# Kernel tuning notes

Measured on AMD Instinct MI355X. Metric: run time of the kernel, lower is better.

Reference implementation:

```python
import jax, jax.numpy as jnp
import numpy as np

N_HEADS = 8
WINDOW = 7

def _conv1x1(x, W, b):
    # x: [B,H,W,C]; 1x1 conv == per-pixel matmul
    return jnp.einsum('bhwc,cd->bhwd', x, W) + b

def _to_heads(t, nh):
    # [B,H,W,C] -> channels-first reshape [B, nh, C//nh, H*W] (matches tf transpose+reshape)
    B, H, W, C = t.shape
    return jnp.transpose(t, (0, 3, 1, 2)).reshape(B, nh, C // nh, H * W)

def setup_inputs() -> dict:
    key = jax.random.key(0)
    ks = jax.random.split(key, 8)
    B, H, W, C = 2, 56, 56, 256
    x = jax.random.normal(ks[0], (B, H, W, C), dtype=jnp.float32)
    s = 1.0 / np.sqrt(C)
    Wq = jax.random.normal(ks[1], (C, C), dtype=jnp.float32) * s
    bq = jnp.zeros((C,), dtype=jnp.float32)
    Wk = jax.random.normal(ks[2], (C, C), dtype=jnp.float32) * s
    bk = jnp.zeros((C,), dtype=jnp.float32)
    Wv = jax.random.normal(ks[3], (C, C), dtype=jnp.float32) * s
    bv = jnp.zeros((C,), dtype=jnp.float32)
    # original initializes gamma to 0 (output == x); use small nonzero so the
    # attention path is observable in outputs/grads
    gamma = jax.random.normal(ks[4], (1,), dtype=jnp.float32) * 0.1
    return {"x": x, "Wq": Wq, "bq": bq, "Wk": Wk, "bk": bk, "Wv": Wv, "bv": bv, "gamma": gamma}

def reference(x, Wq, bq, Wk, bk, Wv, bv, gamma):
    B, H, W, C = x.shape
    p = WINDOW // 2
    xp = jnp.pad(x, ((0, 0), (p, p), (p, p), (0, 0)), mode='reflect')  # [B,Hp,Wp,C]
    q = _to_heads(_conv1x1(x, Wq, bq), N_HEADS)    # [B,nh,dk,HW]
    k = _to_heads(_conv1x1(xp, Wk, bk), N_HEADS)   # [B,nh,dk,HpWp]
    v = _to_heads(_conv1x1(xp, Wv, bv), N_HEADS)   # [B,nh,dk,HpWp]
    energy = jnp.einsum('bhdq,bhdk->bhqk', q, k)   # [B,nh,HW,HpWp]
    attn = jax.nn.softmax(energy, axis=-1)
    out = jnp.einsum('bhdk,bhqk->bhdq', v, attn)   # [B,nh,dk,HW]
    out = out.reshape(B, C, H, W).transpose(0, 2, 3, 1)
    return gamma * out + x
```

## Files before the change

kernel.cpp:

```cpp
#include <hip/hip_runtime.h>

typedef unsigned short u16;
typedef float f32x4 __attribute__((ext_vector_type(4)));
typedef short bf16x8 __attribute__((ext_vector_type(8)));
typedef u16 u16x4 __attribute__((ext_vector_type(4)));

__device__ __forceinline__ u16 f2bf(float f) {
    unsigned u = __float_as_uint(f);
    u = (u + 0x7FFFu + ((u >> 16) & 1u)) >> 16;
    return (u16)u;
}

#define LOG2E 1.4426950408889634f

#if __has_builtin(__builtin_amdgcn_exp2f)
__device__ __forceinline__ float exp2_fast(float x) { return __builtin_amdgcn_exp2f(x); }
#else
__device__ __forceinline__ float exp2_fast(float x) { return __expf(x * 0.6931471805599453f); }
#endif

__device__ __forceinline__ unsigned pack2bf(float a, float b) {
    unsigned ua = __float_as_uint(a) + 0x8000u;
    unsigned ub = __float_as_uint(b) + 0x8000u;
#if __has_builtin(__builtin_amdgcn_perm)
    return __builtin_amdgcn_perm(ub, ua, 0x07060302u);
#else
    return ((ua >> 16) & 0xFFFFu) | (ub & 0xFFFF0000u);
#endif
}

#if __has_builtin(__builtin_amdgcn_cvt_pk_bf16_f32)
typedef __bf16 bf2_t __attribute__((ext_vector_type(2)));
__device__ __forceinline__ unsigned cvtpk(float a, float b) {
    bf2_t r = __builtin_amdgcn_cvt_pk_bf16_f32(a, b);
    return __builtin_bit_cast(unsigned, r);
}
#else
__device__ __forceinline__ unsigned cvtpk(float a, float b) { return pack2bf(a, b); }
#endif

__device__ __forceinline__ bf16x8 bc8(uint4 u) { return __builtin_bit_cast(bf16x8, u); }

#if __has_builtin(__builtin_amdgcn_global_load_lds)
typedef const __attribute__((address_space(1))) void* as1cv;
typedef __attribute__((address_space(3))) void* as3v;
__device__ __forceinline__ void dma16(const void* g, void* lds_base, int lane) {
    __builtin_amdgcn_global_load_lds((as1cv)g, (as3v)lds_base, 16, 0, 0);
}
#else
__device__ __forceinline__ void dma16(const void* g, void* lds_base, int lane) {
    *(uint4*)((char*)lds_base + lane * 16) = *(const uint4*)g;
}
#endif

#define BB 2
#define HH 56
#define SQ 3136
#define SKP 3200
#define VT_STRIDE 3200
#define CROWN 3584

#define WS_Q    0
#define WS_K    1605632
#define WS_VT   3211264
#define WS_WT   4849664
#define WS_CB   5046272

__global__ __launch_bounds__(256) void wprep_kernel(const float* __restrict__ Wq,
                                                    const float* __restrict__ Wk,
                                                    const float* __restrict__ Wv,
                                                    u16* __restrict__ wtf,
                                                    u16* __restrict__ vtb,
                                                    u16* __restrict__ crow) {
    __shared__ u16 T[64][68];
    int mode = blockIdx.z;
    const float* W = (mode == 0) ? Wq : ((mode == 1) ? Wk : Wv);
    float sc = (mode == 0) ? LOG2E : 1.0f;
    int kx = blockIdx.x * 64, dx = blockIdx.y * 64;
    int tid = threadIdx.x;
    int r16 = tid >> 4, c4 = (tid & 15) * 4;
#pragma unroll
    for (int p = 0; p < 4; ++p) {
        int kr = p * 16 + r16;
        float4 f = *(const float4*)&W[(size_t)(kx + kr) * 256 + dx + c4];
        T[kr][c4 + 0] = f2bf(f.x * sc);
        T[kr][c4 + 1] = f2bf(f.y * sc);
        T[kr][c4 + 2] = f2bf(f.z * sc);
        T[kr][c4 + 3] = f2bf(f.w * sc);
    }
    __syncthreads();
    int l16 = tid & 15, nt_loc = (tid >> 4) & 3, quad = (tid >> 6) & 3;
#pragma unroll
    for (int s_loc = 0; s_loc < 2; ++s_loc) {
        int k0 = s_loc * 32 + quad * 8;
        int d_loc = nt_loc * 16 + l16;
        u16 tmp[8];
#pragma unroll
        for (int j = 0; j < 8; ++j) tmp[j] = T[k0 + j][d_loc];
        int d = dx + d_loc;
        int nz = d >> 7, ntg = (d >> 4) & 7;
        int s = (kx >> 5) + s_loc;
        int f = (nz * 8 + s) * 8 + ntg;
        int L = quad * 16 + l16;
        *(uint4*)&wtf[(size_t)mode * 65536 + (size_t)f * 512 + (size_t)L * 8] = *(uint4*)tmp;
    }
    if (mode == 1 && kx == 0 && dx == 0) {
        for (int i = tid; i < CROWN; i += 256) {
            u16 v = 0;
            if (i < SQ) {
                int rr = i / 56, cc = i - rr * 56;
                int mr = (((rr >= 1) && (rr <= 3)) || ((rr >= 52) && (rr <= 54))) ? 2 : 1;
                int mc = (((cc >= 1) && (cc <= 3)) || ((cc >= 52) && (cc <= 54))) ? 2 : 1;
                int prod = mr * mc;
                v = (prod == 1) ? (u16)0x3F80 : ((prod == 2) ? (u16)0x4000 : (u16)0x4080);
            }
            crow[i] = v;
        }
    }
    if (mode == 2 && kx == 0 && dx == 0) {
        for (int i = tid; i < 512 * 8; i += 256) {
            int row = i >> 3, c16 = i & 7;
            *(uint4*)&vtb[(size_t)row * VT_STRIDE + SQ + c16 * 8] = (uint4){0, 0, 0, 0};
        }
    }
}

__global__ __launch_bounds__(256, 4) void proj_kernel(const float* __restrict__ x,
                                                      const u16* __restrict__ wtf,
                                                      const float* __restrict__ bq,
                                                      const float* __restrict__ bk,
                                                      const float* __restrict__ bv,
                                                      u16* __restrict__ qout,
                                                      u16* __restrict__ kout,
                                                      u16* __restrict__ vtout) {
    int mode = blockIdx.y, nz = blockIdx.z;
    int mbase = blockIdx.x * 64;
    int tid = threadIdx.x;
    int wave = tid >> 6, quad = (tid >> 4) & 3, l16 = tid & 15;
    const float* bias = (mode == 0) ? bq : ((mode == 1) ? bk : bv);
    float wsc = (mode == 0) ? LOG2E : 1.0f;
    const u16* wf = wtf + (size_t)mode * 65536 + (size_t)nz * 32768 + (size_t)(quad * 16 + l16) * 8;

    int m_a = mbase + wave * 16 + l16;
    const float* xr = x + (size_t)m_a * 256;

    f32x4 acc[8];
#pragma unroll
    for (int i = 0; i < 8; i++) acc[i] = (f32x4){0.f, 0.f, 0.f, 0.f};

#pragma unroll
    for (int s = 0; s < 8; ++s) {
        float4 f0 = *(const float4*)&xr[s * 32 + quad * 8];
        float4 f1 = *(const float4*)&xr[s * 32 + quad * 8 + 4];
        uint4 aw = (uint4){pack2bf(f0.x, f0.y), pack2bf(f0.z, f0.w),
                           pack2bf(f1.x, f1.y), pack2bf(f1.z, f1.w)};
        bf16x8 af = bc8(aw);
        if (mode == 2) {
#pragma unroll
            for (int nt = 0; nt < 8; nt++) {
                bf16x8 bfrag = *(const bf16x8*)&wf[(s * 8 + nt) * 512];
                acc[nt] = __builtin_amdgcn_mfma_f32_16x16x32_bf16(af, bfrag, acc[nt], 0, 0, 0);
            }
        } else {
#pragma unroll
            for (int nt = 0; nt < 8; nt++) {
                bf16x8 bfrag = *(const bf16x8*)&wf[(s * 8 + nt) * 512];
                acc[nt] = __builtin_amdgcn_mfma_f32_16x16x32_bf16(bfrag, af, acc[nt], 0, 0, 0);
            }
        }
    }

    if (mode == 2) {
        int mrow_base = mbase + wave * 16 + quad * 4;
        float mult[4];
#pragma unroll
        for (int p = 0; p < 4; ++p) {
            int m = mrow_base + p;
            int kp = (m >= SQ) ? m - SQ : m;
            int rr = kp / 56, cc = kp - rr * 56;
            float mr = (((rr >= 1) && (rr <= 3)) || ((rr >= 52) && (rr <= 54))) ? 2.f : 1.f;
            float mc = (((cc >= 1) && (cc <= 3)) || ((cc >= 52) && (cc <= 54))) ? 2.f : 1.f;
            mult[p] = mr * mc;
        }
#pragma unroll
        for (int nt = 0; nt < 8; nt++) {
            int c = nz * 128 + nt * 16 + l16;
            float bvv = bias[c];
#pragma unroll
            for (int p = 0; p < 4; p += 2) {
                int m = mrow_base + p;
                int bb = (m >= SQ) ? 1 : 0;
                int kp = m - bb * SQ;
                unsigned pk = pack2bf((acc[nt][p] + bvv) * mult[p],
                                      (acc[nt][p + 1] + bvv) * mult[p + 1]);
                *(unsigned*)&vtout[(size_t)(bb * 256 + c) * VT_STRIDE + kp] = pk;
            }
        }
    } else {
        u16* outp = (mode == 0) ? qout : kout;
#pragma unroll
        for (int nt = 0; nt < 8; nt++) {
            int c0 = nz * 128 + nt * 16 + quad * 4;
            float4 b4 = *(const float4*)&bias[c0];
            float v0 = acc[nt][0] + b4.x * wsc;
            float v1 = acc[nt][1] + b4.y * wsc;
            float v2 = acc[nt][2] + b4.z * wsc;
            float v3 = acc[nt][3] + b4.w * wsc;
            uint2 pk = (uint2){pack2bf(v0, v1), pack2bf(v2, v3)};
            *(uint2*)&outp[((size_t)m_a << 8) + c0] = pk;
        }
    }
}

__global__ __launch_bounds__(256, 4) void attn_kernel(const u16* __restrict__ qb,
                                                      const u16* __restrict__ kb,
                                                      const u16* __restrict__ vtb,
                                                      const u16* __restrict__ crow,
                                                      const float* __restrict__ x,
                                                      const float* __restrict__ gammap,
                                                      float* __restrict__ out) {
    __shared__ __align__(16) u16 S[19968];

    int tid = threadIdx.x;
    int th = tid >> 6, lane = tid & 63, quad = lane >> 4, l16 = lane & 15;
    int bh = blockIdx.x;
    int b = bh >> 3, h = bh & 7;
    int qsub = blockIdx.y * 64;

    bf16x8 qf[4];
#pragma unroll
    for (int i = 0; i < 4; ++i)
        qf[i] = *(const bf16x8*)&qb[((size_t)(b * SQ + qsub + i * 16 + l16) << 8) + h * 32 + quad * 8];

    const u16* kg = kb + ((size_t)(b * SQ) << 8) + h * 32;
    const u16* vg = vtb + (size_t)(b * 256 + h * 32) * VT_STRIDE;

    f32x4 o[4][2], lv[4];
#pragma unroll
    for (int i = 0; i < 4; ++i) {
        o[i][0] = (f32x4){0.f, 0.f, 0.f, 0.f};
        o[i][1] = (f32x4){0.f, 0.f, 0.f, 0.f};
        lv[i]   = (f32x4){0.f, 0.f, 0.f, 0.f};
    }

    auto stage = [&](int r_ch, int buf) {
        u16* base = &S[buf * 8192];
        int kbase = r_ch * 128;
#pragma unroll
        for (int i = 0; i < 2; ++i) {
            int g = th + i * 4;
            int grow = kbase + g * 16 + (lane & 15);
            if (grow > SQ - 1) grow = SQ - 1;
            dma16(kg + ((size_t)grow << 8) + (lane >> 4) * 8, base + g * 512, lane);
            int col = kbase + (2 * g + (lane >> 5)) * 8;
            dma16(vg + (size_t)(lane & 31) * VT_STRIDE + col, base + 4096 + g * 512, lane);
        }
    };

    int tA = th, tB = th + 4;
    int vOffA = tA * 512 + (((quad >> 1) * 32 + l16) << 3) + (quad & 1) * 4;
    int vOffB = tB * 512 + (((quad >> 1) * 32 + l16) << 3) + (quad & 1) * 4;

    auto round_body = [&](int r, int bR) {
        const u16* Kl = &S[bR * 8192];
        const u16* Vl = Kl + 4096;
        const u16* cnt = &S[16384] + r * 128;
        bf16x8 kfA = *(const bf16x8*)&Kl[tA * 512 + lane * 8];
        bf16x8 kfB = *(const bf16x8*)&Kl[tB * 512 + lane * 8];
        uint2 ca = *(const uint2*)&cnt[tA * 16 + quad * 4];
        uint2 cc = *(const uint2*)&cnt[tB * 16 + quad * 4];
        bf16x8 cf = bc8((uint4){ca.x, ca.y, cc.x, cc.y});
        uint2 wA0 = *(const uint2*)&Vl[vOffA];
        uint2 wB0 = *(const uint2*)&Vl[vOffB];
        uint2 wA1 = *(const uint2*)&Vl[vOffA + 128];
        uint2 wB1 = *(const uint2*)&Vl[vOffB + 128];
        bf16x8 V0 = bc8((uint4){wA0.x, wA0.y, wB0.x, wB0.y});
        bf16x8 V1 = bc8((uint4){wA1.x, wA1.y, wB1.x, wB1.y});

        f32x4 z = (f32x4){0.f, 0.f, 0.f, 0.f};
        f32x4 eA[4], eB[4];
#pragma unroll
        for (int i = 0; i < 4; ++i)
            eA[i] = __builtin_amdgcn_mfma_f32_16x16x32_bf16(kfA, qf[i], z, 0, 0, 0);
#pragma unroll
        for (int i = 0; i < 4; ++i)
            eB[i] = __builtin_amdgcn_mfma_f32_16x16x32_bf16(kfB, qf[i], z, 0, 0, 0);

#pragma unroll
        for (int i = 0; i < 4; ++i) {
            float pA0 = exp2_fast(eA[i][0]), pA1 = exp2_fast(eA[i][1]);
            float pA2 = exp2_fast(eA[i][2]), pA3 = exp2_fast(eA[i][3]);
            float pB0 = exp2_fast(eB[i][0]), pB1 = exp2_fast(eB[i][1]);
            float pB2 = exp2_fast(eB[i][2]), pB3 = exp2_fast(eB[i][3]);
            bf16x8 pa = bc8((uint4){cvtpk(pA0, pA1), cvtpk(pA2, pA3),
                                    cvtpk(pB0, pB1), cvtpk(pB2, pB3)});
            o[i][0] = __builtin_amdgcn_mfma_f32_16x16x32_bf16(pa, V0, o[i][0], 0, 0, 0);
            o[i][1] = __builtin_amdgcn_mfma_f32_16x16x32_bf16(pa, V1, o[i][1], 0, 0, 0);
            lv[i]   = __builtin_amdgcn_mfma_f32_16x16x32_bf16(pa, cf, lv[i], 0, 0, 0);
        }
    };

    {
#pragma unroll
        for (int e = 0; e < 2; ++e) {
            int chn = th * 2 + e;
            if (chn < 7)
                dma16(crow + chn * 512 + lane * 8, (char*)&S[16384] + chn * 1024, lane);
        }
    }
    stage(0, 0);
    __syncthreads();

    for (int r = 0; r < 25; ++r) {
        if (r + 1 < 25) {
            stage(r + 1, (r + 1) & 1);
            asm volatile("s_waitcnt vmcnt(4)" ::: "memory");
        } else {
            asm volatile("s_waitcnt vmcnt(0)" ::: "memory");
        }
        round_body(r, r & 1);
    }

    __syncthreads();

    float* mg = (float*)&S[0];
    {
        int slot = ((th & 1) * 64 + lane) * 48;
        if (th >= 2) {
#pragma unroll
            for (int i = 0; i < 4; ++i) {
                *(f32x4*)&mg[slot + i * 8]      = o[i][0];
                *(f32x4*)&mg[slot + i * 8 + 4]  = o[i][1];
                *(f32x4*)&mg[slot + 32 + i * 4] = lv[i];
            }
        }
        __syncthreads();
        if (th < 2) {
#pragma unroll
            for (int i = 0; i < 4; ++i) {
                o[i][0] += *(const f32x4*)&mg[slot + i * 8];
                o[i][1] += *(const f32x4*)&mg[slot + i * 8 + 4];
                lv[i]   += *(const f32x4*)&mg[slot + 32 + i * 4];
            }
        }
        __syncthreads();
    }
    {
        int slot = lane * 48;
        if (th == 1) {
#pragma unroll
            for (int i = 0; i < 4; ++i) {
                *(f32x4*)&mg[slot + i * 8]      = o[i][0];
                *(f32x4*)&mg[slot + i * 8 + 4]  = o[i][1];
                *(f32x4*)&mg[slot + 32 + i * 4] = lv[i];
            }
        }
        __syncthreads();
        if (th == 0) {
            float g = gammap[0];
#pragma unroll
            for (int i = 0; i < 4; ++i) {
                o[i][0] += *(const f32x4*)&mg[slot + i * 8];
                o[i][1] += *(const f32x4*)&mg[slot + i * 8 + 4];
                lv[i]   += *(const f32x4*)&mg[slot + 32 + i * 4];
#pragma unroll
                for (int r2 = 0; r2 < 4; ++r2) {
                    float scl = g / lv[i][r2];
                    int q = qsub + i * 16 + quad * 4 + r2;
                    size_t base = ((size_t)(b * SQ + q) << 8) + h * 32 + l16;
                    out[base]      = o[i][0][r2] * scl + x[base];
                    out[base + 16] = o[i][1][r2] * scl + x[base + 16];
                }
            }
        }
    }
}

extern "C" void kernel_launch(void* const* d_in, const int* in_sizes, int n_in,
                              void* d_out, int out_size, void* d_ws, size_t ws_size,
                              hipStream_t stream) {
    const float* x     = (const float*)d_in[0];
    const float* Wq    = (const float*)d_in[1];
    const float* bq    = (const float*)d_in[2];
    const float* Wk    = (const float*)d_in[3];
    const float* bk    = (const float*)d_in[4];
    const float* Wv    = (const float*)d_in[5];
    const float* bv    = (const float*)d_in[6];
    const float* gamma = (const float*)d_in[7];
    float* out = (float*)d_out;

    u16* ws   = (u16*)d_ws;
    u16* qbuf = ws + WS_Q;
    u16* kbuf = ws + WS_K;
    u16* vtb  = ws + WS_VT;
    u16* wtf  = ws + WS_WT;
    u16* crow = ws + WS_CB;

    wprep_kernel<<<dim3(4, 4, 3), 256, 0, stream>>>(Wq, Wk, Wv, wtf, vtb, crow);
    proj_kernel<<<dim3(98, 3, 2), 256, 0, stream>>>(x, wtf, bq, bk, bv, qbuf, kbuf, vtb);
    attn_kernel<<<dim3(16, 49), 256, 0, stream>>>(qbuf, kbuf, vtb, crow, x, gamma, out);
}
```

Baseline: 150.1 us.

## Pre-convert x to bf16, stage weights in LDS, widen attention blocks to 512 threads

Adds an xprep kernel that converts x to bf16 once, so the projection kernel loads bf16 fragments directly instead of converting fp32 on every load. The projection kernel now stages its weight tile in LDS and splits the output channels across twice as many blocks. The attention kernel doubles block size to 512 threads, with two query halves per block, and each wave stages one K/V chunk per round behind a barrier instead of the earlier vmcnt(4) overlap. This trades an extra kernel launch and more barriers for more parallelism and lower register pressure per wave.

```diff
diff --git a/kernel.cpp b/kernel.cpp
--- a/kernel.cpp
+++ b/kernel.cpp
@@ -3,7 +3,6 @@
 typedef unsigned short u16;
 typedef float f32x4 __attribute__((ext_vector_type(4)));
 typedef short bf16x8 __attribute__((ext_vector_type(8)));
-typedef u16 u16x4 __attribute__((ext_vector_type(4)));
 
 __device__ __forceinline__ u16 f2bf(float f) {
     unsigned u = __float_as_uint(f);
@@ -65,6 +64,18 @@
 #define WS_VT   3211264
 #define WS_WT   4849664
 #define WS_CB   5046272
+#define WS_XB   5049856
+
+__global__ __launch_bounds__(256) void xprep_kernel(const float* __restrict__ x,
+                                                    u16* __restrict__ xb) {
+    int gid = blockIdx.x * 256 + threadIdx.x;
+    const float* src = x + (size_t)gid * 8;
+    float4 f0 = *(const float4*)src;
+    float4 f1 = *(const float4*)(src + 4);
+    uint4 pk = (uint4){pack2bf(f0.x, f0.y), pack2bf(f0.z, f0.w),
+                       pack2bf(f1.x, f1.y), pack2bf(f1.z, f1.w)};
+    *(uint4*)&xb[(size_t)gid * 8] = pk;
+}
 
 __global__ __launch_bounds__(256) void wprep_kernel(const float* __restrict__ Wq,
                                                     const float* __restrict__ Wk,
@@ -125,7 +136,7 @@
     }
 }
 
-__global__ __launch_bounds__(256, 4) void proj_kernel(const float* __restrict__ x,
+__global__ __launch_bounds__(256, 5) void proj_kernel(const u16* __restrict__ xb,
                                                       const u16* __restrict__ wtf,
                                                       const float* __restrict__ bq,
                                                       const float* __restrict__ bk,
@@ -133,41 +144,50 @@
                                                       u16* __restrict__ qout,
                                                       u16* __restrict__ kout,
                                                       u16* __restrict__ vtout) {
-    int mode = blockIdx.y, nz = blockIdx.z;
+    __shared__ __align__(16) u16 Bl[16384];
+    int mode = blockIdx.y, nz2 = blockIdx.z;
     int mbase = blockIdx.x * 64;
     int tid = threadIdx.x;
-    int wave = tid >> 6, quad = (tid >> 4) & 3, l16 = tid & 15;
+    int wave = tid >> 6, lane = tid & 63, quad = (tid >> 4) & 3, l16 = tid & 15;
+    int nz = nz2 >> 1, hi = nz2 & 1;
     const float* bias = (mode == 0) ? bq : ((mode == 1) ? bk : bv);
     float wsc = (mode == 0) ? LOG2E : 1.0f;
-    const u16* wf = wtf + (size_t)mode * 65536 + (size_t)nz * 32768 + (size_t)(quad * 16 + l16) * 8;
-
+    const u16* wbase = wtf + (size_t)mode * 65536 + (size_t)nz * 32768 + hi * 2048;
+
+#pragma unroll
+    for (int j = 0; j < 8; ++j) {
+        int fi = wave * 8 + j;
+        int s = fi >> 2, nt = fi & 3;
+        dma16(wbase + s * 4096 + nt * 512 + lane * 8, (char*)Bl + fi * 1024, lane);
+    }
     int m_a = mbase + wave * 16 + l16;
-    const float* xr = x + (size_t)m_a * 256;
-
-    f32x4 acc[8];
-#pragma unroll
-    for (int i = 0; i < 8; i++) acc[i] = (f32x4){0.f, 0.f, 0.f, 0.f};
-
-#pragma unroll
-    for (int s = 0; s < 8; ++s) {
-        float4 f0 = *(const float4*)&xr[s * 32 + quad * 8];
-        float4 f1 = *(const float4*)&xr[s * 32 + quad * 8 + 4];
-        uint4 aw = (uint4){pack2bf(f0.x, f0.y), pack2bf(f0.z, f0.w),
-                           pack2bf(f1.x, f1.y), pack2bf(f1.z, f1.w)};
-        bf16x8 af = bc8(aw);
-        if (mode == 2) {
-#pragma unroll
-            for (int nt = 0; nt < 8; nt++) {
-                bf16x8 bfrag = *(const bf16x8*)&wf[(s * 8 + nt) * 512];
-                acc[nt] = __builtin_amdgcn_mfma_f32_16x16x32_bf16(af, bfrag, acc[nt], 0, 0, 0);
+    const u16* xr = xb + ((size_t)m_a << 8);
+    bf16x8 aa[8];
+#pragma unroll
+    for (int s = 0; s < 8; ++s)
+        aa[s] = *(const bf16x8*)&xr[s * 32 + quad * 8];
+    __syncthreads();
+
+    f32x4 acc[4];
+#pragma unroll
+    for (int i = 0; i < 4; i++) acc[i] = (f32x4){0.f, 0.f, 0.f, 0.f};
+
+    if (mode == 2) {
+#pragma unroll
+        for (int s = 0; s < 8; ++s)
+#pragma unroll
+            for (int nt = 0; nt < 4; ++nt) {
+                bf16x8 bf = *(const bf16x8*)&Bl[(s * 4 + nt) * 512 + lane * 8];
+                acc[nt] = __builtin_amdgcn_mfma_f32_16x16x32_bf16(aa[s], bf, acc[nt], 0, 0, 0);
             }
-        } else {
-#pragma unroll
-            for (int nt = 0; nt < 8; nt++) {
-                bf16x8 bfrag = *(const bf16x8*)&wf[(s * 8 + nt) * 512];
-                acc[nt] = __builtin_amdgcn_mfma_f32_16x16x32_bf16(bfrag, af, acc[nt], 0, 0, 0);
+    } else {
+#pragma unroll
+        for (int s = 0; s < 8; ++s)
+#pragma unroll
+            for (int nt = 0; nt < 4; ++nt) {
+                bf16x8 bf = *(const bf16x8*)&Bl[(s * 4 + nt) * 512 + lane * 8];
+                acc[nt] = __builtin_amdgcn_mfma_f32_16x16x32_bf16(bf, aa[s], acc[nt], 0, 0, 0);
             }
-        }
     }
 
     if (mode == 2) {
@@ -183,8 +203,8 @@
             mult[p] = mr * mc;
         }
 #pragma unroll
-        for (int nt = 0; nt < 8; nt++) {
-            int c = nz * 128 + nt * 16 + l16;
+        for (int nt = 0; nt < 4; nt++) {
+            int c = nz2 * 64 + nt * 16 + l16;
             float bvv = bias[c];
 #pragma unroll
             for (int p = 0; p < 4; p += 2) {
@@ -199,8 +219,8 @@
     } else {
         u16* outp = (mode == 0) ? qout : kout;
 #pragma unroll
-        for (int nt = 0; nt < 8; nt++) {
-            int c0 = nz * 128 + nt * 16 + quad * 4;
+        for (int nt = 0; nt < 4; nt++) {
+            int c0 = nz2 * 64 + nt * 16 + quad * 4;
             float4 b4 = *(const float4*)&bias[c0];
             float v0 = acc[nt][0] + b4.x * wsc;
             float v1 = acc[nt][1] + b4.y * wsc;
@@ -212,7 +232,7 @@
     }
 }
 
-__global__ __launch_bounds__(256, 4) void attn_kernel(const u16* __restrict__ qb,
+__global__ __launch_bounds__(512, 8) void attn_kernel(const u16* __restrict__ qb,
                                                       const u16* __restrict__ kb,
                                                       const u16* __restrict__ vtb,
                                                       const u16* __restrict__ crow,
@@ -222,22 +242,23 @@
     __shared__ __align__(16) u16 S[19968];
 
     int tid = threadIdx.x;
-    int th = tid >> 6, lane = tid & 63, quad = lane >> 4, l16 = lane & 15;
+    int w = tid >> 6, lane = tid & 63, quad = lane >> 4, l16 = lane & 15;
+    int g = w & 3, qh = w >> 2;
     int bh = blockIdx.x;
     int b = bh >> 3, h = bh & 7;
-    int qsub = blockIdx.y * 64;
-
-    bf16x8 qf[4];
-#pragma unroll
-    for (int i = 0; i < 4; ++i)
-        qf[i] = *(const bf16x8*)&qb[((size_t)(b * SQ + qsub + i * 16 + l16) << 8) + h * 32 + quad * 8];
+    int qbase = b * SQ + blockIdx.y * 64 + qh * 32;
+
+    bf16x8 qf[2];
+#pragma unroll
+    for (int i = 0; i < 2; ++i)
+        qf[i] = *(const bf16x8*)&qb[((size_t)(qbase + i * 16 + l16) << 8) + h * 32 + quad * 8];
 
     const u16* kg = kb + ((size_t)(b * SQ) << 8) + h * 32;
     const u16* vg = vtb + (size_t)(b * 256 + h * 32) * VT_STRIDE;
 
-    f32x4 o[4][2], lv[4];
-#pragma unroll
-    for (int i = 0; i < 4; ++i) {
+    f32x4 o[2][2], lv[2];
+#pragma unroll
+    for (int i = 0; i < 2; ++i) {
         o[i][0] = (f32x4){0.f, 0.f, 0.f, 0.f};
         o[i][1] = (f32x4){0.f, 0.f, 0.f, 0.f};
         lv[i]   = (f32x4){0.f, 0.f, 0.f, 0.f};
@@ -246,18 +267,14 @@
     auto stage = [&](int r_ch, int buf) {
         u16* base = &S[buf * 8192];
         int kbase = r_ch * 128;
-#pragma unroll
-        for (int i = 0; i < 2; ++i) {
-            int g = th + i * 4;
-            int grow = kbase + g * 16 + (lane & 15);
-            if (grow > SQ - 1) grow = SQ - 1;
-            dma16(kg + ((size_t)grow << 8) + (lane >> 4) * 8, base + g * 512, lane);
-            int col = kbase + (2 * g + (lane >> 5)) * 8;
-            dma16(vg + (size_t)(lane & 31) * VT_STRIDE + col, base + 4096 + g * 512, lane);
-        }
+        int grow = kbase + w * 16 + l16;
+        if (grow > SQ - 1) grow = SQ - 1;
+        dma16(kg + ((size_t)grow << 8) + (lane >> 4) * 8, base + w * 512, lane);
+        int col = kbase + (2 * w + (lane >> 5)) * 8;
+        dma16(vg + (size_t)(lane & 31) * VT_STRIDE + col, base + 4096 + w * 512, lane);
     };
 
-    int tA = th, tB = th + 4;
+    int tA = g, tB = g + 4;
     int vOffA = tA * 512 + (((quad >> 1) * 32 + l16) << 3) + (quad & 1) * 4;
     int vOffB = tB * 512 + (((quad >> 1) * 32 + l16) << 3) + (quad & 1) * 4;
 
@@ -278,16 +295,16 @@
         bf16x8 V1 = bc8((uint4){wA1.x, wA1.y, wB1.x, wB1.y});
 
         f32x4 z = (f32x4){0.f, 0.f, 0.f, 0.f};
-        f32x4 eA[4], eB[4];
-#pragma unroll
-        for (int i = 0; i < 4; ++i)
+        f32x4 eA[2], eB[2];
+#pragma unroll
+        for (int i = 0; i < 2; ++i)
             eA[i] = __builtin_amdgcn_mfma_f32_16x16x32_bf16(kfA, qf[i], z, 0, 0, 0);
 #pragma unroll
-        for (int i = 0; i < 4; ++i)
+        for (int i = 0; i < 2; ++i)
             eB[i] = __builtin_amdgcn_mfma_f32_16x16x32_bf16(kfB, qf[i], z, 0, 0, 0);
 
 #pragma unroll
-        for (int i = 0; i < 4; ++i) {
+        for (int i = 0; i < 2; ++i) {
             float pA0 = exp2_fast(eA[i][0]), pA1 = exp2_fast(eA[i][1]);
             float pA2 = exp2_fast(eA[i][2]), pA3 = exp2_fast(eA[i][3]);
             float pB0 = exp2_fast(eB[i][0]), pB1 = exp2_fast(eB[i][1]);
@@ -300,73 +317,65 @@
         }
     };
 
-    {
-#pragma unroll
-        for (int e = 0; e < 2; ++e) {
-            int chn = th * 2 + e;
-            if (chn < 7)
-                dma16(crow + chn * 512 + lane * 8, (char*)&S[16384] + chn * 1024, lane);
-        }
-    }
+    if (w < 7) dma16(crow + w * 512 + lane * 8, (char*)&S[16384] + w * 1024, lane);
     stage(0, 0);
-    __syncthreads();
 
     for (int r = 0; r < 25; ++r) {
-        if (r + 1 < 25) {
-            stage(r + 1, (r + 1) & 1);
-            asm volatile("s_waitcnt vmcnt(4)" ::: "memory");
-        } else {
-            asm volatile("s_waitcnt vmcnt(0)" ::: "memory");
-        }
+        asm volatile("s_waitcnt vmcnt(0)" ::: "memory");
+        __builtin_amdgcn_s_barrier();
+        asm volatile("" ::: "memory");
+        if (r + 1 < 25) stage(r + 1, (r + 1) & 1);
         round_body(r, r & 1);
     }
-
     __syncthreads();
 
     float* mg = (float*)&S[0];
     {
-        int slot = ((th & 1) * 64 + lane) * 48;
-        if (th >= 2) {
-#pragma unroll
-            for (int i = 0; i < 4; ++i) {
-                *(f32x4*)&mg[slot + i * 8]      = o[i][0];
-                *(f32x4*)&mg[slot + i * 8 + 4]  = o[i][1];
-                *(f32x4*)&mg[slot + 32 + i * 4] = lv[i];
-            }
+        int slot = ((qh * 2 + (g & 1)) * 64 + lane) * 24;
+        if (g >= 2) {
+            *(f32x4*)&mg[slot + 0]  = o[0][0];
+            *(f32x4*)&mg[slot + 4]  = o[0][1];
+            *(f32x4*)&mg[slot + 8]  = o[1][0];
+            *(f32x4*)&mg[slot + 12] = o[1][1];
+            *(f32x4*)&mg[slot + 16] = lv[0];
+            *(f32x4*)&mg[slot + 20] = lv[1];
         }
         __syncthreads();
-        if (th < 2) {
-#pragma unroll
-            for (int i = 0; i < 4; ++i) {
-                o[i][0] += *(const f32x4*)&mg[slot + i * 8];
-                o[i][1] += *(const f32x4*)&mg[slot + i * 8 + 4];
-                lv[i]   += *(const f32x4*)&mg[slot + 32 + i * 4];
-            }
+        if (g < 2) {
+            o[0][0] += *(const f32x4*)&mg[slot + 0];
+            o[0][1] += *(const f32x4*)&mg[slot + 4];
+            o[1][0] += *(const f32x4*)&mg[slot + 8];
+            o[1][1] += *(const f32x4*)&mg[slot + 12];
+            lv[0]   += *(const f32x4*)&mg[slot + 16];
+            lv[1]   += *(const f32x4*)&mg[slot + 20];
         }
         __syncthreads();
     }
     {
-        int slot = lane * 48;
-        if (th == 1) {
-#pragma unroll
-            for (int i = 0; i < 4; ++i) {
-                *(f32x4*)&mg[slot + i * 8]      = o[i][0];
-                *(f32x4*)&mg[slot + i * 8 + 4]  = o[i][1];
-                *(f32x4*)&mg[slot + 32 + i * 4] = lv[i];
-            }
+        int slot = (qh * 64 + lane) * 24;
+        if (g == 1) {
+            *(f32x4*)&mg[slot + 0]  = o[0][0];
+            *(f32x4*)&mg[slot + 4]  = o[0][1];
+            *(f32x4*)&mg[slot + 8]  = o[1][0];
+            *(f32x4*)&mg[slot + 12] = o[1][1];
+            *(f32x4*)&mg[slot + 16] = lv[0];
+            *(f32x4*)&mg[slot + 20] = lv[1];
         }
         __syncthreads();
-        if (th == 0) {
-            float g = gammap[0];
-#pragma unroll
-            for (int i = 0; i < 4; ++i) {
-                o[i][0] += *(const f32x4*)&mg[slot + i * 8];
-                o[i][1] += *(const f32x4*)&mg[slot + i * 8 + 4];
-                lv[i]   += *(const f32x4*)&mg[slot + 32 + i * 4];
+        if (g == 0) {
+            o[0][0] += *(const f32x4*)&mg[slot + 0];
+            o[0][1] += *(const f32x4*)&mg[slot + 4];
+            o[1][0] += *(const f32x4*)&mg[slot + 8];
+            o[1][1] += *(const f32x4*)&mg[slot + 12];
+            lv[0]   += *(const f32x4*)&mg[slot + 16];
+            lv[1]   += *(const f32x4*)&mg[slot + 20];
+            float gam = gammap[0];
+#pragma unroll
+            for (int i = 0; i < 2; ++i) {
 #pragma unroll
                 for (int r2 = 0; r2 < 4; ++r2) {
-                    float scl = g / lv[i][r2];
-                    int q = qsub + i * 16 + quad * 4 + r2;
+                    float scl = gam / lv[i][r2];
+                    int q = blockIdx.y * 64 + qh * 32 + i * 16 + quad * 4 + r2;
                     size_t base = ((size_t)(b * SQ + q) << 8) + h * 32 + l16;
                     out[base]      = o[i][0][r2] * scl + x[base];
                     out[base + 16] = o[i][1][r2] * scl + x[base + 16];
@@ -395,8 +404,10 @@
     u16* vtb  = ws + WS_VT;
     u16* wtf  = ws + WS_WT;
     u16* crow = ws + WS_CB;
-
+    u16* xb   = ws + WS_XB;
+
+    xprep_kernel<<<784, 256, 0, stream>>>(x, xb);
     wprep_kernel<<<dim3(4, 4, 3), 256, 0, stream>>>(Wq, Wk, Wv, wtf, vtb, crow);
-    proj_kernel<<<dim3(98, 3, 2), 256, 0, stream>>>(x, wtf, bq, bk, bv, qbuf, kbuf, vtb);
-    attn_kernel<<<dim3(16, 49), 256, 0, stream>>>(qbuf, kbuf, vtb, crow, x, gamma, out);
-}
+    proj_kernel<<<dim3(98, 3, 4), 256, 0, stream>>>(xb, wtf, bq, bk, bv, qbuf, kbuf, vtb);
+    attn_kernel<<<dim3(16, 49), 512, 0, stream>>>(qbuf, kbuf, vtb, crow, x, gamma, out);
+}
```

Measured after the change: 236.1 us. +57.3%, slower.
